# Optimization experiments

Hardware: AMD Instinct MI355X
Metric: run time of the kernel (lower is better)

Reference implementation:

```python
import jax, jax.numpy as jnp
import numpy as np

N_LAYERS = 4
GAMMA = 0.5
D_MODEL = 256
D_STATE = 64
D_CONV = 4
EXPAND = 2
D_INNER = EXPAND * D_MODEL            # 512 (= headdim, so nheads = 1)
NHEADS = 1
CONV_DIM = D_INNER + 2 * D_STATE      # 640
D_IN_PROJ = 2 * D_INNER + 2 * D_STATE + NHEADS  # 1153
VOCAB = 100
VOCAB_PAD = 104                        # padded to multiple of 8 by MambaConfig
BATCH = 8
SEQ = 2048


def setup_inputs() -> dict:
    key = jax.random.key(0)
    ks = jax.random.split(key, 8)
    def nrm(k, shape):
        # gamma init: std = 1 / d1**gamma, d1 = shape[0]
        return (jax.random.normal(k, shape, jnp.float32) * (1.0 / shape[0] ** GAMMA))
    inp = {}
    inp["input_ids"] = jax.random.randint(ks[0], (BATCH, SEQ), 0, VOCAB)
    inp["embed"] = nrm(ks[1], (VOCAB_PAD, D_MODEL))          # tied embedding / lm_head
    inp["in_proj_w"] = nrm(ks[2], (N_LAYERS * D_IN_PROJ, D_MODEL)).reshape(N_LAYERS, D_IN_PROJ, D_MODEL)
    inp["conv_w"] = nrm(ks[3], (N_LAYERS * CONV_DIM, D_CONV)).reshape(N_LAYERS, CONV_DIM, D_CONV)
    inp["conv_b"] = jnp.zeros((N_LAYERS, CONV_DIM), jnp.float32)
    inp["dt_bias"] = jax.random.uniform(ks[4], (N_LAYERS, NHEADS), jnp.float32, -4.0, -1.0)
    inp["A_log"] = jnp.log(jax.random.uniform(ks[5], (N_LAYERS, NHEADS), jnp.float32, 1.0, 16.0))
    inp["Dparam"] = jnp.ones((N_LAYERS, NHEADS), jnp.float32)
    inp["norm_g_w"] = jnp.ones((N_LAYERS, D_INNER), jnp.float32)
    inp["out_proj_w"] = nrm(ks[6], (N_LAYERS * D_MODEL, D_INNER)).reshape(N_LAYERS, D_MODEL, D_INNER)
    inp["block_norm_w"] = jnp.ones((N_LAYERS, D_MODEL), jnp.float32)
    inp["norm_f_w"] = jnp.ones((D_MODEL,), jnp.float32)
    return inp


def rmsnorm(x, w, eps=1e-5):
    return x * jax.lax.rsqrt(jnp.mean(x * x, axis=-1, keepdims=True) + eps) * w


def ssm_scan(x, dt, A, Bc, Cc):
    # x: (B,L,P)  dt: (B,L)  A: scalar  Bc,Cc: (B,L,N). Sequential selective scan.
    def step(h, inp):  # h: (B,P,N)
        x_t, dt_t, b_t, c_t = inp
        h = h * jnp.exp(dt_t * A)[:, None, None] + (dt_t[:, None] * x_t)[:, :, None] * b_t[:, None, :]
        y = jnp.einsum('bpn,bn->bp', h, c_t)
        return h, y
    h0 = jnp.zeros((x.shape[0], x.shape[2], Bc.shape[2]), x.dtype)
    xs = (jnp.swapaxes(x, 0, 1), jnp.swapaxes(dt, 0, 1), jnp.swapaxes(Bc, 0, 1), jnp.swapaxes(Cc, 0, 1))
    _, ys = jax.lax.scan(step, h0, xs)
    return jnp.swapaxes(ys, 0, 1)  # (B,L,P)


def mamba2_mixer(h, ipw, cw, cb, dtb, alog, dp, ngw, opw):
    zxbcdt = h @ ipw.T                                   # (B,L,1153)
    z = zxbcdt[..., :D_INNER]
    xBC = zxbcdt[..., D_INNER:D_INNER + CONV_DIM]
    dt_raw = zxbcdt[..., D_INNER + CONV_DIM:]            # (B,L,1)
    # depthwise causal conv1d (kernel D_CONV) + SiLU
    xp = jnp.pad(xBC, ((0, 0), (D_CONV - 1, 0), (0, 0)))
    L = xBC.shape[1]
    conv = sum(xp[:, k:k + L, :] * cw[:, k] for k in range(D_CONV)) + cb
    xBC = jax.nn.silu(conv)
    x = xBC[..., :D_INNER]
    Bc = xBC[..., D_INNER:D_INNER + D_STATE]
    Cc = xBC[..., D_INNER + D_STATE:]
    dt = jax.nn.softplus(dt_raw[..., 0] + dtb[0])        # (B,L), nheads=1
    A = -jnp.exp(alog[0])
    y = ssm_scan(x, dt, A, Bc, Cc) + dp[0] * x
    y = rmsnorm(y * jax.nn.silu(z), ngw)                 # RMSNormGated (norm after gate)
    return y @ opw.T


def reference(input_ids, embed, in_proj_w, conv_w, conv_b, dt_bias, A_log, Dparam,
              norm_g_w, out_proj_w, block_norm_w, norm_f_w):
    hidden = embed[input_ids]                            # (B,L,D_MODEL)
    residual = None
    for i in range(N_LAYERS):
        residual = hidden if residual is None else hidden + residual
        hidden = rmsnorm(residual, block_norm_w[i])
        hidden = mamba2_mixer(hidden, in_proj_w[i], conv_w[i], conv_b[i], dt_bias[i],
                              A_log[i], Dparam[i], norm_g_w[i], out_proj_w[i])
    residual = hidden + residual
    final = rmsnorm(residual, norm_f_w)
    logits = final @ embed.T                             # tied lm_head, (B,L,VOCAB_PAD)
    return logits[:, -1, :VOCAB]                         # last-token logits, (B,VOCAB)
```

## Files before the change

### kernel.cpp

```cpp
#include <hip/hip_runtime.h>
#include <math.h>

#define NB    8
#define LSEQ  2048
#define TKN   16384
#define DM    256
#define DI    512
#define DS    64
#define DIP   1153
#define DIPP  1160
#define CDIM  640
#define NL    4
#define NC    16
#define CL    128
#define VOC   100

typedef short bf16x8 __attribute__((ext_vector_type(8)));
typedef short bf16x4 __attribute__((ext_vector_type(4)));
typedef float f32x4  __attribute__((ext_vector_type(4)));
typedef unsigned short ushort_t;

__device__ __forceinline__ float block_reduce_sum256(float v) {
  __shared__ float sred[4];
  #pragma unroll
  for (int off = 32; off > 0; off >>= 1) v += __shfl_down(v, off, 64);
  int lane = threadIdx.x & 63, wid = threadIdx.x >> 6;
  if (lane == 0) sred[wid] = v;
  __syncthreads();
  return sred[0] + sred[1] + sred[2] + sred[3];
}

__device__ __forceinline__ unsigned short f2bf(float f) {
  unsigned int u = __float_as_uint(f);
  unsigned int r = u + 0x7FFFu + ((u >> 16) & 1u);
  return (unsigned short)(r >> 16);
}
__device__ __forceinline__ float bf2f(unsigned short u) {
  return __uint_as_float(((unsigned int)u) << 16);
}

__global__ __launch_bounds__(256) void convert_w(const float* __restrict__ ipw,
    const float* __restrict__ opw, ushort_t* __restrict__ wbi, ushort_t* __restrict__ wbo) {
  const int n1 = NL * DIP * DM;
  const int n2 = NL * DM * DI;
  int i4 = (blockIdx.x * 256 + threadIdx.x) * 4;
  if (i4 < n1) {
    float4 v = *(const float4*)(ipw + i4);
    bf16x4 o; o[0] = (short)f2bf(v.x); o[1] = (short)f2bf(v.y);
    o[2] = (short)f2bf(v.z); o[3] = (short)f2bf(v.w);
    *(bf16x4*)(wbi + i4) = o;
  } else {
    int j = i4 - n1;
    if (j < n2) {
      float4 v = *(const float4*)(opw + j);
      bf16x4 o; o[0] = (short)f2bf(v.x); o[1] = (short)f2bf(v.y);
      o[2] = (short)f2bf(v.z); o[3] = (short)f2bf(v.w);
      *(bf16x4*)(wbo + j) = o;
    }
  }
}

__global__ __launch_bounds__(256) void embed_init(const int* __restrict__ ids,
    const float* __restrict__ embed, float* __restrict__ mixo, float* __restrict__ resid) {
  int t = blockIdx.x, tid = threadIdx.x;
  int id = ids[t];
  mixo[(size_t)t * DM + tid] = embed[(size_t)id * DM + tid];
  resid[(size_t)t * DM + tid] = 0.f;
}

__global__ __launch_bounds__(256) void add_rmsnorm(float* __restrict__ resid,
    const float* __restrict__ mixo, ushort_t* __restrict__ hn, const float* __restrict__ w) {
  int wave = threadIdx.x >> 6, lane = threadIdx.x & 63;
  int t = blockIdx.x * 4 + wave;
  size_t o = (size_t)t * DM + lane * 4;
  float4 r4 = *(const float4*)&resid[o];
  float4 m4 = *(const float4*)&mixo[o];
  r4.x += m4.x; r4.y += m4.y; r4.z += m4.z; r4.w += m4.w;
  *(float4*)&resid[o] = r4;
  float ss = r4.x * r4.x + r4.y * r4.y + r4.z * r4.z + r4.w * r4.w;
  #pragma unroll
  for (int m = 32; m >= 1; m >>= 1) ss += __shfl_xor(ss, m, 64);
  float sc = rsqrtf(ss * (1.f / DM) + 1e-5f);
  float4 w4 = *(const float4*)&w[lane * 4];
  bf16x4 o4;
  o4[0] = (short)f2bf(r4.x * sc * w4.x);
  o4[1] = (short)f2bf(r4.y * sc * w4.y);
  o4[2] = (short)f2bf(r4.z * sc * w4.z);
  o4[3] = (short)f2bf(r4.w * sc * w4.w);
  *(bf16x4*)&hn[o] = o4;
}

#define LSTR 40
template<typename TC>
__global__ __launch_bounds__(256) void gemm_nt_bf16(const ushort_t* __restrict__ A,
    const ushort_t* __restrict__ Bw, TC* __restrict__ C, int N, int K, int ldc) {
  __shared__ short sA[128 * LSTR];
  __shared__ short sB[128 * LSTR];
  int tid = threadIdx.x;
  int bn = blockIdx.x * 128;
  int bm = blockIdx.y * 128;
  int wave = tid >> 6, lane = tid & 63;
  int wm = (wave >> 1) * 64, wn = (wave & 1) * 64;
  int q = lane >> 4, c = lane & 15;

  f32x4 acc[4][4];
  #pragma unroll
  for (int i = 0; i < 4; ++i)
    #pragma unroll
    for (int j = 0; j < 4; ++j) acc[i][j] = (f32x4)0.f;

  int sr = tid >> 1;
  int sc = (tid & 1) * 16;
  const ushort_t* Ag = A + (size_t)(bm + sr) * K + sc;
  const ushort_t* Bg = Bw + (size_t)(bn + sr) * K + sc;
  bool bok = (bn + sr) < N;
  short* sAp = &sA[sr * LSTR + sc];
  short* sBp = &sB[sr * LSTR + sc];

  for (int k0 = 0; k0 < K; k0 += 32) {
    bf16x8 a0 = *(const bf16x8*)(Ag + k0);
    bf16x8 a1 = *(const bf16x8*)(Ag + k0 + 8);
    bf16x8 b0 = (bf16x8)(short)0, b1 = (bf16x8)(short)0;
    if (bok) {
      b0 = *(const bf16x8*)(Bg + k0);
      b1 = *(const bf16x8*)(Bg + k0 + 8);
    }
    __syncthreads();
    *(bf16x8*)(sAp)     = a0;
    *(bf16x8*)(sAp + 8) = a1;
    *(bf16x8*)(sBp)     = b0;
    *(bf16x8*)(sBp + 8) = b1;
    __syncthreads();
    bf16x8 af[4], bfr[4];
    #pragma unroll
    for (int i = 0; i < 4; ++i)
      af[i] = *(const bf16x8*)&sA[(wm + i * 16 + c) * LSTR + q * 8];
    #pragma unroll
    for (int j = 0; j < 4; ++j)
      bfr[j] = *(const bf16x8*)&sB[(wn + j * 16 + c) * LSTR + q * 8];
    #pragma unroll
    for (int i = 0; i < 4; ++i)
      #pragma unroll
      for (int j = 0; j < 4; ++j)
        acc[i][j] = __builtin_amdgcn_mfma_f32_16x16x32_bf16(af[i], bfr[j], acc[i][j], 0, 0, 0);
  }
  #pragma unroll
  for (int i = 0; i < 4; ++i) {
    int m = bm + wm + i * 16 + q * 4;
    #pragma unroll
    for (int j = 0; j < 4; ++j) {
      int n = bn + wn + j * 16 + c;
      if (n < N) {
        #pragma unroll
        for (int r = 0; r < 4; ++r) {
          if constexpr (sizeof(TC) == 2)
            C[(size_t)(m + r) * ldc + n] = (TC)f2bf(acc[i][j][r]);
          else
            C[(size_t)(m + r) * ldc + n] = acc[i][j][r];
        }
      }
    }
  }
}

__global__ __launch_bounds__(256) void outproj_fused(const ushort_t* __restrict__ yb,
    const ushort_t* __restrict__ zx, const ushort_t* __restrict__ Bw,
    const float* __restrict__ gw, float* __restrict__ Cout) {
  __shared__ short sA[64 * LSTR];
  __shared__ short sB[128 * LSTR];
  __shared__ float swl[DI];
  __shared__ float rs[256];
  int tid = threadIdx.x;
  int bn = blockIdx.x * 128;
  int bm = blockIdx.y * 64;
  int wave = tid >> 6, lane = tid & 63;
  int wm = (wave >> 1) * 32, wn = (wave & 1) * 64;
  int q = lane >> 4, c = lane & 15;
  swl[tid] = gw[tid];
  swl[tid + 256] = gw[tid + 256];

  f32x4 acc[2][4];
  #pragma unroll
  for (int i = 0; i < 2; ++i)
    #pragma unroll
    for (int j = 0; j < 4; ++j) acc[i][j] = (f32x4)0.f;

  int ar = tid >> 2, ak = (tid & 3) * 8;
  int br = tid >> 1, bk = (tid & 1) * 16;
  const ushort_t* yrow = yb + (size_t)(bm + ar) * DI + ak;
  const ushort_t* zrow = zx + (size_t)(bm + ar) * DIPP + ak;
  const ushort_t* Bg = Bw + (size_t)(bn + br) * DI + bk;
  short* sAp = &sA[ar * LSTR + ak];
  short* sBp = &sB[br * LSTR + bk];
  float sumsq = 0.f;
  __syncthreads();

  for (int k0 = 0; k0 < DI; k0 += 32) {
    bf16x8 y8 = *(const bf16x8*)(yrow + k0);
    bf16x8 z8 = *(const bf16x8*)(zrow + k0);
    bf16x8 b0 = *(const bf16x8*)(Bg + k0);
    bf16x8 b1 = *(const bf16x8*)(Bg + k0 + 8);
    bf16x8 g8;
    #pragma unroll
    for (int e = 0; e < 8; ++e) {
      float zz = bf2f((ushort_t)z8[e]);
      float gg = bf2f((ushort_t)y8[e]) * (zz / (1.f + __expf(-zz)));
      sumsq += gg * gg;
      g8[e] = (short)f2bf(gg * swl[k0 + ak + e]);
    }
    __syncthreads();
    *(bf16x8*)(sAp)     = g8;
    *(bf16x8*)(sBp)     = b0;
    *(bf16x8*)(sBp + 8) = b1;
    __syncthreads();
    bf16x8 af[2], bfr[4];
    #pragma unroll
    for (int i = 0; i < 2; ++i)
      af[i] = *(const bf16x8*)&sA[(wm + i * 16 + c) * LSTR + q * 8];
    #pragma unroll
    for (int j = 0; j < 4; ++j)
      bfr[j] = *(const bf16x8*)&sB[(wn + j * 16 + c) * LSTR + q * 8];
    #pragma unroll
    for (int i = 0; i < 2; ++i)
      #pragma unroll
      for (int j = 0; j < 4; ++j)
        acc[i][j] = __builtin_amdgcn_mfma_f32_16x16x32_bf16(af[i], bfr[j], acc[i][j], 0, 0, 0);
  }
  rs[tid] = sumsq;
  __syncthreads();
  #pragma unroll
  for (int i = 0; i < 2; ++i) {
    #pragma unroll
    for (int r = 0; r < 4; ++r) {
      int ml = wm + i * 16 + q * 4 + r;
      float rtot = rs[ml * 4] + rs[ml * 4 + 1] + rs[ml * 4 + 2] + rs[ml * 4 + 3];
      float scale = rsqrtf(rtot * (1.f / DI) + 1e-5f);
      #pragma unroll
      for (int j = 0; j < 4; ++j) {
        int n = bn + wn + j * 16 + c;
        Cout[(size_t)(bm + ml) * DM + n] = scale * acc[i][j][r];
      }
    }
  }
}

__global__ __launch_bounds__(256) void conv_silu(const ushort_t* __restrict__ zx,
    const float* __restrict__ cw, const float* __restrict__ cb,
    const float* __restrict__ dtb, ushort_t* __restrict__ xo,
    ushort_t* __restrict__ Bo, ushort_t* __restrict__ Co, ushort_t* __restrict__ Ut) {
  __shared__ ushort_t tile[67 * 128];
  __shared__ ushort_t tt[128 * 65];
  __shared__ float sdt[64];
  int tid = threadIdx.x;
  int ct = blockIdx.x, tb_ = blockIdx.y, b = blockIdx.z;
  int c0 = ct * 128, l0 = tb_ * 64;
  size_t rowb = (size_t)b * LSEQ;
  bool isx = (ct < 4);
  for (int slot = tid; slot < 67 * 16; slot += 256) {
    int r = slot >> 4, gg = slot & 15;
    int l = l0 + r - 3;
    bf16x8 v = (bf16x8)(short)0;
    if (l >= 0) v = *(const bf16x8*)&zx[(rowb + l) * DIPP + DI + c0 + gg * 8];
    *(bf16x8*)&tile[r * 128 + gg * 8] = v;
  }
  if (isx && tid < 64) sdt[tid] = dtb[rowb + l0 + tid];
  int g = tid & 15, tq = tid >> 4;
  int cbase = c0 + g * 8;
  float w[4][8], bias[8];
  #pragma unroll
  for (int e = 0; e < 8; ++e) {
    float4 wv = *(const float4*)&cw[(cbase + e) * 4];
    w[0][e] = wv.x; w[1][e] = wv.y; w[2][e] = wv.z; w[3][e] = wv.w;
    bias[e] = cb[cbase + e];
  }
  __syncthreads();
  bf16x8 rows[7];
  #pragma unroll
  for (int r = 0; r < 7; ++r)
    rows[r] = *(const bf16x8*)&tile[(tq * 4 + r) * 128 + g * 8];
  #pragma unroll
  for (int it = 0; it < 4; ++it) {
    int t = tq * 4 + it;
    size_t tl = rowb + l0 + t;
    float dtv = isx ? sdt[t] : 0.f;
    bf16x8 o;
    #pragma unroll
    for (int e = 0; e < 8; ++e) {
      float s = bias[e]
              + w[0][e] * bf2f((ushort_t)rows[it][e])
              + w[1][e] * bf2f((ushort_t)rows[it + 1][e])
              + w[2][e] * bf2f((ushort_t)rows[it + 2][e])
              + w[3][e] * bf2f((ushort_t)rows[it + 3][e]);
      float v = s / (1.f + __expf(-s));
      o[e] = (short)f2bf(v);
      if (isx) tt[(g * 8 + e) * 65 + t] = f2bf(v * dtv);
    }
    if (isx) {
      *(bf16x8*)&xo[tl * DI + cbase] = o;
    } else if (g < 8) {
      *(bf16x8*)&Bo[tl * DS + (cbase - DI)] = o;
    } else {
      *(bf16x8*)&Co[tl * DS + (cbase - DI - DS)] = o;
    }
  }
  if (isx) {
    __syncthreads();
    int os = tid & 63;
    #pragma unroll
    for (int pass = 0; pass < 32; ++pass) {
      int op = (tid >> 6) + pass * 4;
      Ut[((size_t)b * DI + c0 + op) * LSEQ + l0 + os] = tt[op * 65 + os];
    }
  }
}

__global__ __launch_bounds__(256) void csum_k(const ushort_t* __restrict__ zx,
    const float* __restrict__ dtbias, float* __restrict__ dtb, float* __restrict__ csumb) {
  int tid = threadIdx.x;
  int wave = tid >> 6, lane = tid & 63;
  int cg = blockIdx.x * 4 + wave;
  int b = cg >> 4, ch = cg & 15;
  size_t base = (size_t)b * LSEQ + ch * CL;
  float bias = dtbias[0];
  float x0 = bf2f(zx[(base + 2 * lane) * DIPP + (DIP - 1)]) + bias;
  float x1 = bf2f(zx[(base + 2 * lane + 1) * DIPP + (DIP - 1)]) + bias;
  float d0 = (x0 > 20.f) ? x0 : log1pf(__expf(x0));
  float d1 = (x1 > 20.f) ? x1 : log1pf(__expf(x1));
  dtb[base + 2 * lane] = d0;
  dtb[base + 2 * lane + 1] = d1;
  float p = d0 + d1;
  #pragma unroll
  for (int off = 1; off < 64; off <<= 1) {
    float t = __shfl_up(p, off, 64);
    if (lane >= off) p += t;
  }
  csumb[base + 2 * lane]     = p - d1;
  csumb[base + 2 * lane + 1] = p;
}

__global__ __launch_bounds__(256) void state_gemm(const ushort_t* __restrict__ Bb,
    const ushort_t* __restrict__ Ut, const float* __restrict__ csumb,
    const float* __restrict__ alog, float* __restrict__ hst) {
  __shared__ short sW[64 * 144];
  __shared__ short sX[128 * 40];
  __shared__ float scs[128];
  int tid = threadIdx.x;
  int ph = blockIdx.x, ch = blockIdx.y, b = blockIdx.z;
  int bc = b * NC + ch;
  size_t tb = (size_t)b * LSEQ + ch * CL;
  float Aval = -expf(alog[0]);
  if (tid < 128) scs[tid] = csumb[tb + tid];
  __syncthreads();
  float Stot = scs[127];
  {
    int s = tid >> 1, noff = (tid & 1) * 32;
    float scale = __expf(Aval * (Stot - scs[s]));
    #pragma unroll
    for (int blk = 0; blk < 4; ++blk) {
      bf16x8 v = *(const bf16x8*)&Bb[(tb + s) * DS + noff + blk * 8];
      #pragma unroll
      for (int e = 0; e < 8; ++e)
        sW[(noff + blk * 8 + e) * 144 + s] = (short)f2bf(bf2f((ushort_t)v[e]) * scale);
    }
  }
  int wave = tid >> 6, lane = tid & 63;
  int wn = (wave >> 1) * 32, wp = (wave & 1) * 64;
  int q = lane >> 4, c = lane & 15;
  f32x4 acc[2][4];
  #pragma unroll
  for (int i = 0; i < 2; ++i)
    #pragma unroll
    for (int j = 0; j < 4; ++j) acc[i][j] = (f32x4)0.f;

  for (int ks = 0; ks < 4; ++ks) {
    __syncthreads();
    {
      int r = tid >> 1, off = (tid & 1) * 16;
      size_t ua = ((size_t)b * DI + ph * 128 + r) * LSEQ + ch * CL + ks * 32 + off;
      bf16x8 u0 = *(const bf16x8*)&Ut[ua];
      bf16x8 u1 = *(const bf16x8*)&Ut[ua + 8];
      *(bf16x8*)&sX[r * 40 + off]     = u0;
      *(bf16x8*)&sX[r * 40 + off + 8] = u1;
    }
    __syncthreads();
    bf16x8 af[2], bfr[4];
    #pragma unroll
    for (int i = 0; i < 2; ++i)
      af[i] = *(const bf16x8*)&sW[(wn + i * 16 + c) * 144 + ks * 32 + q * 8];
    #pragma unroll
    for (int j = 0; j < 4; ++j)
      bfr[j] = *(const bf16x8*)&sX[(wp + j * 16 + c) * 40 + q * 8];
    #pragma unroll
    for (int i = 0; i < 2; ++i)
      #pragma unroll
      for (int j = 0; j < 4; ++j)
        acc[i][j] = __builtin_amdgcn_mfma_f32_16x16x32_bf16(af[i], bfr[j], acc[i][j], 0, 0, 0);
  }
  #pragma unroll
  for (int i = 0; i < 2; ++i) {
    int n = wn + i * 16 + q * 4;
    #pragma unroll
    for (int j = 0; j < 4; ++j) {
      int pg = ph * 128 + wp + j * 16 + c;
      #pragma unroll
      for (int r = 0; r < 4; ++r)
        hst[((size_t)bc * DS + n + r) * DI + pg] = acc[i][j][r];
    }
  }
}

__global__ __launch_bounds__(256) void combine2(const float* __restrict__ hst,
    const float* __restrict__ csumb, const float* __restrict__ alog,
    ushort_t* __restrict__ hin) {
  __shared__ ushort_t ts[64 * 17];
  int tid = threadIdx.x;
  int pt = blockIdx.x, nt = blockIdx.y, b = blockIdx.z;
  int p0 = pt * 64, n0 = nt * 16;
  int pl = tid & 63, ng = tid >> 6;
  float Aval = -expf(alog[0]);
  float h[4];
  #pragma unroll
  for (int i = 0; i < 4; ++i) h[i] = 0.f;
  for (int c = 0; c < NC; ++c) {
    int bc = b * NC + c;
    #pragma unroll
    for (int i = 0; i < 4; ++i)
      ts[pl * 17 + ng * 4 + i] = f2bf(h[i]);
    __syncthreads();
    {
      int on = tid & 15;
      #pragma unroll
      for (int pass = 0; pass < 4; ++pass) {
        int op = (tid >> 4) + pass * 16;
        hin[((size_t)bc * DI + p0 + op) * DS + n0 + on] = ts[op * 17 + on];
      }
    }
    __syncthreads();
    float Sc = csumb[(size_t)b * LSEQ + c * CL + CL - 1];
    float dec = __expf(Aval * Sc);
    #pragma unroll
    for (int i = 0; i < 4; ++i) {
      float loc = hst[((size_t)bc * DS + n0 + ng * 4 + i) * DI + p0 + pl];
      h[i] = h[i] * dec + loc;
    }
  }
}

__global__ __launch_bounds__(256) void y_gemm(const ushort_t* __restrict__ Bb,
    const ushort_t* __restrict__ Cb, const ushort_t* __restrict__ Ut,
    const ushort_t* __restrict__ hin, const float* __restrict__ csumb,
    const float* __restrict__ alog, const float* __restrict__ dpar,
    const ushort_t* __restrict__ xb, ushort_t* __restrict__ y) {
  __shared__ short sC[128 * 72];
  __shared__ short sM[128 * 136];
  __shared__ short sU[128 * 80];
  __shared__ float scs[128];
  int tid = threadIdx.x;
  int ph = blockIdx.x, ch = blockIdx.y, b = blockIdx.z;
  int bc = b * NC + ch;
  size_t tb = (size_t)b * LSEQ + ch * CL;
  float Aval = -expf(alog[0]);
  float dp = dpar[0];
  int wave = tid >> 6, lane = tid & 63;
  int q = lane >> 4, c = lane & 15;

  {
    int r = tid >> 1, off = (tid & 1) * 32;
    #pragma unroll
    for (int blk = 0; blk < 4; ++blk) {
      *(bf16x8*)&sC[r * 72 + off + blk * 8] = *(const bf16x8*)&Cb[(tb + r) * DS + off + blk * 8];
      *(bf16x8*)&sU[r * 80 + off + blk * 8] = *(const bf16x8*)&Bb[(tb + r) * DS + off + blk * 8];
    }
  }
  if (tid < 128) scs[tid] = csumb[tb + tid];
  __syncthreads();

  {
    int wm = (wave >> 1) * 64, wss = (wave & 1) * 64;
    f32x4 g[4][4];
    #pragma unroll
    for (int i = 0; i < 4; ++i)
      #pragma unroll
      for (int j = 0; j < 4; ++j) g[i][j] = (f32x4)0.f;
    #pragma unroll
    for (int k0 = 0; k0 < 64; k0 += 32) {
      bf16x8 af[4], bfr[4];
      #pragma unroll
      for (int i = 0; i < 4; ++i)
        af[i] = *(const bf16x8*)&sC[(wm + i * 16 + c) * 72 + k0 + q * 8];
      #pragma unroll
      for (int j = 0; j < 4; ++j)
        bfr[j] = *(const bf16x8*)&sU[(wss + j * 16 + c) * 80 + k0 + q * 8];
      #pragma unroll
      for (int i = 0; i < 4; ++i)
        #pragma unroll
        for (int j = 0; j < 4; ++j)
          g[i][j] = __builtin_amdgcn_mfma_f32_16x16x32_bf16(af[i], bfr[j], g[i][j], 0, 0, 0);
    }
    #pragma unroll
    for (int i = 0; i < 4; ++i) {
      #pragma unroll
      for (int r = 0; r < 4; ++r) {
        int t = wm + i * 16 + q * 4 + r;
        float ct = scs[t];
        #pragma unroll
        for (int j = 0; j < 4; ++j) {
          int s = wss + j * 16 + c;
          float v = g[i][j][r];
          float m = (s <= t) ? v * __expf(Aval * (ct - scs[s])) : 0.f;
          sM[t * 136 + s] = (short)f2bf(m);
        }
      }
    }
  }

  int wm2 = (wave >> 1) * 64, wp = (wave & 1) * 64;
  f32x4 acc[4][4];
  #pragma unroll
  for (int i = 0; i < 4; ++i)
    #pragma unroll
    for (int j = 0; j < 4; ++j) acc[i][j] = (f32x4)0.f;

  for (int ks = 0; ks < 4; ++ks) {
    __syncthreads();
    {
      int r = tid >> 1, off = (tid & 1) * 16;
      size_t ua = ((size_t)b * DI + ph * 128 + r) * LSEQ + ch * CL + ks * 32 + off;
      bf16x8 u0 = *(const bf16x8*)&Ut[ua];
      bf16x8 u1 = *(const bf16x8*)&Ut[ua + 8];
      *(bf16x8*)&sU[r * 40 + off]     = u0;
      *(bf16x8*)&sU[r * 40 + off + 8] = u1;
    }
    __syncthreads();
    bf16x8 af[4], bfr[4];
    #pragma unroll
    for (int i = 0; i < 4; ++i)
      af[i] = *(const bf16x8*)&sM[(wm2 + i * 16 + c) * 136 + ks * 32 + q * 8];
    #pragma unroll
    for (int j = 0; j < 4; ++j)
      bfr[j] = *(const bf16x8*)&sU[(wp + j * 16 + c) * 40 + q * 8];
    #pragma unroll
    for (int i = 0; i < 4; ++i)
      #pragma unroll
      for (int j = 0; j < 4; ++j)
        acc[i][j] = __builtin_amdgcn_mfma_f32_16x16x32_bf16(af[i], bfr[j], acc[i][j], 0, 0, 0);
  }

  __syncthreads();
  {
    int r = tid >> 1, off = (tid & 1) * 32;
    float sc_t = __expf(Aval * scs[r]);
    #pragma unroll
    for (int blk = 0; blk < 4; ++blk) {
      bf16x8 v = *(const bf16x8*)&sC[r * 72 + off + blk * 8];
      bf16x8 o;
      #pragma unroll
      for (int e = 0; e < 8; ++e)
        o[e] = (short)f2bf(bf2f((ushort_t)v[e]) * sc_t);
      *(bf16x8*)&sM[r * 80 + off + blk * 8] = o;
    }
  }
  for (int ks = 4; ks < 6; ++ks) {
    __syncthreads();
    {
      int r = tid >> 1, off = (tid & 1) * 16;
      size_t ha = ((size_t)bc * DI + ph * 128 + r) * DS + (ks - 4) * 32 + off;
      bf16x8 h0 = *(const bf16x8*)&hin[ha];
      bf16x8 h1 = *(const bf16x8*)&hin[ha + 8];
      *(bf16x8*)&sU[r * 40 + off]     = h0;
      *(bf16x8*)&sU[r * 40 + off + 8] = h1;
    }
    __syncthreads();
    bf16x8 af[4], bfr[4];
    #pragma unroll
    for (int i = 0; i < 4; ++i)
      af[i] = *(const bf16x8*)&sM[(wm2 + i * 16 + c) * 80 + (ks - 4) * 32 + q * 8];
    #pragma unroll
    for (int j = 0; j < 4; ++j)
      bfr[j] = *(const bf16x8*)&sU[(wp + j * 16 + c) * 40 + q * 8];
    #pragma unroll
    for (int i = 0; i < 4; ++i)
      #pragma unroll
      for (int j = 0; j < 4; ++j)
        acc[i][j] = __builtin_amdgcn_mfma_f32_16x16x32_bf16(af[i], bfr[j], acc[i][j], 0, 0, 0);
  }

  #pragma unroll
  for (int i = 0; i < 4; ++i) {
    #pragma unroll
    for (int r = 0; r < 4; ++r) {
      int t = wm2 + i * 16 + q * 4 + r;
      size_t row = (tb + t) * DI;
      #pragma unroll
      for (int j = 0; j < 4; ++j) {
        int pg = ph * 128 + wp + j * 16 + c;
        y[row + pg] = f2bf(acc[i][j][r] + dp * bf2f(xb[row + pg]));
      }
    }
  }
}

__global__ __launch_bounds__(256) void finalize(const float* __restrict__ resid,
    const float* __restrict__ mixo, const float* __restrict__ embed,
    const float* __restrict__ nfw, float* __restrict__ out) {
  int b = blockIdx.x, tid = threadIdx.x;
  __shared__ float fin[DM];
  size_t off = ((size_t)b * LSEQ + (LSEQ - 1)) * DM;
  float r = resid[off + tid] + mixo[off + tid];
  float ss = block_reduce_sum256(r * r);
  fin[tid] = r * rsqrtf(ss * (1.f / DM) + 1e-5f) * nfw[tid];
  __syncthreads();
  if (tid < VOC) {
    float acc = 0.f;
    #pragma unroll 8
    for (int d = 0; d < DM; ++d) acc += fin[d] * embed[(size_t)tid * DM + d];
    out[b * VOC + tid] = acc;
  }
}

extern "C" void kernel_launch(void* const* d_in, const int* in_sizes, int n_in,
                              void* d_out, int out_size, void* d_ws, size_t ws_size,
                              hipStream_t stream) {
  const int*   ids   = (const int*)d_in[0];
  const float* embed = (const float*)d_in[1];
  const float* ipw   = (const float*)d_in[2];
  const float* cw    = (const float*)d_in[3];
  const float* cb    = (const float*)d_in[4];
  const float* dtbias= (const float*)d_in[5];
  const float* alog  = (const float*)d_in[6];
  const float* dpar  = (const float*)d_in[7];
  const float* ngw   = (const float*)d_in[8];
  const float* opw   = (const float*)d_in[9];
  const float* bnw   = (const float*)d_in[10];
  const float* nfw   = (const float*)d_in[11];
  float* out = (float*)d_out;

  char* p = (char*)d_ws;
  float* resid = (float*)p;            p += (size_t)TKN * DM * 4;
  float* mixo  = (float*)p;            p += (size_t)TKN * DM * 4;
  ushort_t* hn = (ushort_t*)p;         p += (size_t)TKN * DM * 2;
  ushort_t* zx = (ushort_t*)p;         p += (size_t)TKN * DIPP * 2;
  float* dtb   = (float*)p;            p += (size_t)TKN * 4;
  float* csumb = (float*)p;            p += (size_t)TKN * 4;
  ushort_t* xb = (ushort_t*)p;         p += (size_t)TKN * DI * 2;
  ushort_t* yb = (ushort_t*)p;         p += (size_t)TKN * DI * 2;
  ushort_t* Bb = (ushort_t*)p;         p += (size_t)TKN * DS * 2;
  ushort_t* Cb = (ushort_t*)p;         p += (size_t)TKN * DS * 2;
  ushort_t* Ut = (ushort_t*)p;         p += (size_t)TKN * DI * 2;
  ushort_t* hin= (ushort_t*)p;         p += (size_t)NB * NC * DI * DS * 2;
  ushort_t* wbi= (ushort_t*)p;         p += (size_t)NL * DIP * DM * 2;
  ushort_t* wbo= (ushort_t*)p;         p += (size_t)NL * DM * DI * 2;
  float* hst = (float*)yb;

  convert_w<<<(NL * DIP * DM + NL * DM * DI + 1023) / 1024, 256, 0, stream>>>(
      ipw, opw, wbi, wbo);
  embed_init<<<TKN, 256, 0, stream>>>(ids, embed, mixo, resid);

  for (int i = 0; i < NL; ++i) {
    add_rmsnorm<<<TKN / 4, 256, 0, stream>>>(resid, mixo, hn, bnw + (size_t)i * DM);
    gemm_nt_bf16<ushort_t><<<dim3((DIP + 127) / 128, TKN / 128), 256, 0, stream>>>(
        hn, wbi + (size_t)i * DIP * DM, zx, DIP, DM, DIPP);
    csum_k<<<32, 256, 0, stream>>>(zx, dtbias + i, dtb, csumb);
    conv_silu<<<dim3(CDIM / 128, LSEQ / 64, NB), 256, 0, stream>>>(
        zx, cw + (size_t)i * CDIM * 4, cb + (size_t)i * CDIM, dtb, xb, Bb, Cb, Ut);
    state_gemm<<<dim3(4, NC, NB), 256, 0, stream>>>(Bb, Ut, csumb, alog + i, hst);
    combine2<<<dim3(DI / 64, 4, NB), 256, 0, stream>>>(hst, csumb, alog + i, hin);
    y_gemm<<<dim3(4, NC, NB), 256, 0, stream>>>(Bb, Cb, Ut, hin, csumb, alog + i,
                                                dpar + i, xb, yb);
    outproj_fused<<<dim3(2, TKN / 64), 256, 0, stream>>>(
        yb, zx, wbo + (size_t)i * DM * DI, ngw + (size_t)i * DI, mixo);
  }

  finalize<<<NB, 256, 0, stream>>>(resid, mixo, embed, nfw, out);
}
```

Baseline: 600.8 us.

## Fuse embedding into first rmsnorm, deepen GEMM k-tile, vectorize transpose, skip masked MFMA

Drops the separate embed_init kernel and gathers embedding rows directly in the first add_rmsnorm pass, which removes one full read and write of the residual buffers. The in_proj GEMM now stages 64-wide K tiles so the loop has half as many barriers. conv_silu pads its transpose buffer and writes Ut with 16-byte vector stores instead of scalar ones. In y_gemm the wave whose block of the causal mask is entirely zero just writes zeros and skips its MFMA work, which leaves that wave's load unbalanced.

```diff
diff --git a/kernel.cpp b/kernel.cpp
--- a/kernel.cpp
+++ b/kernel.cpp
@@ -60,22 +60,21 @@
   }
 }
 
-__global__ __launch_bounds__(256) void embed_init(const int* __restrict__ ids,
-    const float* __restrict__ embed, float* __restrict__ mixo, float* __restrict__ resid) {
-  int t = blockIdx.x, tid = threadIdx.x;
-  int id = ids[t];
-  mixo[(size_t)t * DM + tid] = embed[(size_t)id * DM + tid];
-  resid[(size_t)t * DM + tid] = 0.f;
-}
-
 __global__ __launch_bounds__(256) void add_rmsnorm(float* __restrict__ resid,
-    const float* __restrict__ mixo, ushort_t* __restrict__ hn, const float* __restrict__ w) {
+    const float* __restrict__ mixo, ushort_t* __restrict__ hn, const float* __restrict__ w,
+    const int* __restrict__ ids, const float* __restrict__ embed, int first) {
   int wave = threadIdx.x >> 6, lane = threadIdx.x & 63;
   int t = blockIdx.x * 4 + wave;
   size_t o = (size_t)t * DM + lane * 4;
-  float4 r4 = *(const float4*)&resid[o];
-  float4 m4 = *(const float4*)&mixo[o];
-  r4.x += m4.x; r4.y += m4.y; r4.z += m4.z; r4.w += m4.w;
+  float4 r4;
+  if (first) {
+    int id = ids[t];
+    r4 = *(const float4*)&embed[(size_t)id * DM + lane * 4];
+  } else {
+    float4 m4 = *(const float4*)&mixo[o];
+    r4 = *(const float4*)&resid[o];
+    r4.x += m4.x; r4.y += m4.y; r4.z += m4.z; r4.w += m4.w;
+  }
   *(float4*)&resid[o] = r4;
   float ss = r4.x * r4.x + r4.y * r4.y + r4.z * r4.z + r4.w * r4.w;
   #pragma unroll
@@ -90,12 +89,13 @@
   *(bf16x4*)&hn[o] = o4;
 }
 
-#define LSTR 40
+#define LSTR  40
+#define LSTR2 72
 template<typename TC>
 __global__ __launch_bounds__(256) void gemm_nt_bf16(const ushort_t* __restrict__ A,
     const ushort_t* __restrict__ Bw, TC* __restrict__ C, int N, int K, int ldc) {
-  __shared__ short sA[128 * LSTR];
-  __shared__ short sB[128 * LSTR];
+  __shared__ short sA[128 * LSTR2];
+  __shared__ short sB[128 * LSTR2];
   int tid = threadIdx.x;
   int bn = blockIdx.x * 128;
   int bm = blockIdx.y * 128;
@@ -110,39 +110,51 @@
     for (int j = 0; j < 4; ++j) acc[i][j] = (f32x4)0.f;
 
   int sr = tid >> 1;
-  int sc = (tid & 1) * 16;
+  int sc = (tid & 1) * 32;
   const ushort_t* Ag = A + (size_t)(bm + sr) * K + sc;
   const ushort_t* Bg = Bw + (size_t)(bn + sr) * K + sc;
   bool bok = (bn + sr) < N;
-  short* sAp = &sA[sr * LSTR + sc];
-  short* sBp = &sB[sr * LSTR + sc];
-
-  for (int k0 = 0; k0 < K; k0 += 32) {
+  short* sAp = &sA[sr * LSTR2 + sc];
+  short* sBp = &sB[sr * LSTR2 + sc];
+
+  for (int k0 = 0; k0 < K; k0 += 64) {
     bf16x8 a0 = *(const bf16x8*)(Ag + k0);
     bf16x8 a1 = *(const bf16x8*)(Ag + k0 + 8);
+    bf16x8 a2 = *(const bf16x8*)(Ag + k0 + 16);
+    bf16x8 a3 = *(const bf16x8*)(Ag + k0 + 24);
     bf16x8 b0 = (bf16x8)(short)0, b1 = (bf16x8)(short)0;
+    bf16x8 b2 = (bf16x8)(short)0, b3 = (bf16x8)(short)0;
     if (bok) {
       b0 = *(const bf16x8*)(Bg + k0);
       b1 = *(const bf16x8*)(Bg + k0 + 8);
-    }
-    __syncthreads();
-    *(bf16x8*)(sAp)     = a0;
-    *(bf16x8*)(sAp + 8) = a1;
-    *(bf16x8*)(sBp)     = b0;
-    *(bf16x8*)(sBp + 8) = b1;
-    __syncthreads();
-    bf16x8 af[4], bfr[4];
-    #pragma unroll
-    for (int i = 0; i < 4; ++i)
-      af[i] = *(const bf16x8*)&sA[(wm + i * 16 + c) * LSTR + q * 8];
-    #pragma unroll
-    for (int j = 0; j < 4; ++j)
-      bfr[j] = *(const bf16x8*)&sB[(wn + j * 16 + c) * LSTR + q * 8];
-    #pragma unroll
-    for (int i = 0; i < 4; ++i)
+      b2 = *(const bf16x8*)(Bg + k0 + 16);
+      b3 = *(const bf16x8*)(Bg + k0 + 24);
+    }
+    __syncthreads();
+    *(bf16x8*)(sAp)      = a0;
+    *(bf16x8*)(sAp + 8)  = a1;
+    *(bf16x8*)(sAp + 16) = a2;
+    *(bf16x8*)(sAp + 24) = a3;
+    *(bf16x8*)(sBp)      = b0;
+    *(bf16x8*)(sBp + 8)  = b1;
+    *(bf16x8*)(sBp + 16) = b2;
+    *(bf16x8*)(sBp + 24) = b3;
+    __syncthreads();
+    #pragma unroll
+    for (int ks = 0; ks < 2; ++ks) {
+      bf16x8 af[4], bfr[4];
+      #pragma unroll
+      for (int i = 0; i < 4; ++i)
+        af[i] = *(const bf16x8*)&sA[(wm + i * 16 + c) * LSTR2 + ks * 32 + q * 8];
       #pragma unroll
       for (int j = 0; j < 4; ++j)
-        acc[i][j] = __builtin_amdgcn_mfma_f32_16x16x32_bf16(af[i], bfr[j], acc[i][j], 0, 0, 0);
+        bfr[j] = *(const bf16x8*)&sB[(wn + j * 16 + c) * LSTR2 + ks * 32 + q * 8];
+      #pragma unroll
+      for (int i = 0; i < 4; ++i)
+        #pragma unroll
+        for (int j = 0; j < 4; ++j)
+          acc[i][j] = __builtin_amdgcn_mfma_f32_16x16x32_bf16(af[i], bfr[j], acc[i][j], 0, 0, 0);
+    }
   }
   #pragma unroll
   for (int i = 0; i < 4; ++i) {
@@ -249,7 +261,7 @@
     const float* __restrict__ dtb, ushort_t* __restrict__ xo,
     ushort_t* __restrict__ Bo, ushort_t* __restrict__ Co, ushort_t* __restrict__ Ut) {
   __shared__ ushort_t tile[67 * 128];
-  __shared__ ushort_t tt[128 * 65];
+  __shared__ ushort_t tt[128 * 72];
   __shared__ float sdt[64];
   int tid = threadIdx.x;
   int ct = blockIdx.x, tb_ = blockIdx.y, b = blockIdx.z;
@@ -293,7 +305,7 @@
               + w[3][e] * bf2f((ushort_t)rows[it + 3][e]);
       float v = s / (1.f + __expf(-s));
       o[e] = (short)f2bf(v);
-      if (isx) tt[(g * 8 + e) * 65 + t] = f2bf(v * dtv);
+      if (isx) tt[(g * 8 + e) * 72 + t] = f2bf(v * dtv);
     }
     if (isx) {
       *(bf16x8*)&xo[tl * DI + cbase] = o;
@@ -305,11 +317,12 @@
   }
   if (isx) {
     __syncthreads();
-    int os = tid & 63;
-    #pragma unroll
-    for (int pass = 0; pass < 32; ++pass) {
-      int op = (tid >> 6) + pass * 4;
-      Ut[((size_t)b * DI + c0 + op) * LSEQ + l0 + os] = tt[op * 65 + os];
+    #pragma unroll
+    for (int pass = 0; pass < 4; ++pass) {
+      int slot = pass * 256 + tid;
+      int op = slot >> 3, sg = slot & 7;
+      bf16x8 v = *(const bf16x8*)&tt[op * 72 + sg * 8];
+      *(bf16x8*)&Ut[((size_t)b * DI + c0 + op) * LSEQ + l0 + sg * 8] = v;
     }
   }
 }
@@ -477,38 +490,51 @@
 
   {
     int wm = (wave >> 1) * 64, wss = (wave & 1) * 64;
-    f32x4 g[4][4];
-    #pragma unroll
-    for (int i = 0; i < 4; ++i)
-      #pragma unroll
-      for (int j = 0; j < 4; ++j) g[i][j] = (f32x4)0.f;
-    #pragma unroll
-    for (int k0 = 0; k0 < 64; k0 += 32) {
-      bf16x8 af[4], bfr[4];
-      #pragma unroll
-      for (int i = 0; i < 4; ++i)
-        af[i] = *(const bf16x8*)&sC[(wm + i * 16 + c) * 72 + k0 + q * 8];
-      #pragma unroll
-      for (int j = 0; j < 4; ++j)
-        bfr[j] = *(const bf16x8*)&sU[(wss + j * 16 + c) * 80 + k0 + q * 8];
+    if (wave == 1) {
+      #pragma unroll
+      for (int i = 0; i < 4; ++i) {
+        #pragma unroll
+        for (int r = 0; r < 4; ++r) {
+          int t = i * 16 + q * 4 + r;
+          #pragma unroll
+          for (int j = 0; j < 4; ++j)
+            sM[t * 136 + 64 + j * 16 + c] = 0;
+        }
+      }
+    } else {
+      f32x4 g[4][4];
       #pragma unroll
       for (int i = 0; i < 4; ++i)
         #pragma unroll
+        for (int j = 0; j < 4; ++j) g[i][j] = (f32x4)0.f;
+      #pragma unroll
+      for (int k0 = 0; k0 < 64; k0 += 32) {
+        bf16x8 af[4], bfr[4];
+        #pragma unroll
+        for (int i = 0; i < 4; ++i)
+          af[i] = *(const bf16x8*)&sC[(wm + i * 16 + c) * 72 + k0 + q * 8];
+        #pragma unroll
         for (int j = 0; j < 4; ++j)
-          g[i][j] = __builtin_amdgcn_mfma_f32_16x16x32_bf16(af[i], bfr[j], g[i][j], 0, 0, 0);
-    }
-    #pragma unroll
-    for (int i = 0; i < 4; ++i) {
-      #pragma unroll
-      for (int r = 0; r < 4; ++r) {
-        int t = wm + i * 16 + q * 4 + r;
-        float ct = scs[t];
+          bfr[j] = *(const bf16x8*)&sU[(wss + j * 16 + c) * 80 + k0 + q * 8];
         #pragma unroll
-        for (int j = 0; j < 4; ++j) {
-          int s = wss + j * 16 + c;
-          float v = g[i][j][r];
-          float m = (s <= t) ? v * __expf(Aval * (ct - scs[s])) : 0.f;
-          sM[t * 136 + s] = (short)f2bf(m);
+        for (int i = 0; i < 4; ++i)
+          #pragma unroll
+          for (int j = 0; j < 4; ++j)
+            g[i][j] = __builtin_amdgcn_mfma_f32_16x16x32_bf16(af[i], bfr[j], g[i][j], 0, 0, 0);
+      }
+      #pragma unroll
+      for (int i = 0; i < 4; ++i) {
+        #pragma unroll
+        for (int r = 0; r < 4; ++r) {
+          int t = wm + i * 16 + q * 4 + r;
+          float ct = scs[t];
+          #pragma unroll
+          for (int j = 0; j < 4; ++j) {
+            int s = wss + j * 16 + c;
+            float v = g[i][j][r];
+            float m = (s <= t) ? v * __expf(Aval * (ct - scs[s])) : 0.f;
+            sM[t * 136 + s] = (short)f2bf(m);
+          }
         }
       }
     }
@@ -654,10 +680,10 @@
 
   convert_w<<<(NL * DIP * DM + NL * DM * DI + 1023) / 1024, 256, 0, stream>>>(
       ipw, opw, wbi, wbo);
-  embed_init<<<TKN, 256, 0, stream>>>(ids, embed, mixo, resid);
 
   for (int i = 0; i < NL; ++i) {
-    add_rmsnorm<<<TKN / 4, 256, 0, stream>>>(resid, mixo, hn, bnw + (size_t)i * DM);
+    add_rmsnorm<<<TKN / 4, 256, 0, stream>>>(resid, mixo, hn, bnw + (size_t)i * DM,
+                                             ids, embed, i == 0 ? 1 : 0);
     gemm_nt_bf16<ushort_t><<<dim3((DIP + 127) / 128, TKN / 128), 256, 0, stream>>>(
         hn, wbi + (size_t)i * DIP * DM, zx, DIP, DM, DIPP);
     csum_k<<<32, 256, 0, stream>>>(zx, dtbias + i, dtb, csumb);
```

New measurement: 580.5 us. -3.4%, faster.
